# Performance work log

Measured on AMD Instinct MI355X. Metric: run time of the kernel, lower is better.

## Reference

```python
import jax, jax.numpy as jnp
import numpy as np

# Problem sizes
B, NPG, K = 64, 1024, 16          # graphs, nodes-per-graph, kNN neighbors
IN_CH, OUT_CH, SPACE, PROP = 64, 128, 4, 64
N = B * NPG


def setup_inputs() -> dict:
    key = jax.random.key(0)
    ks = jax.random.split(key, 10)

    def lin(k, out_d, in_d):
        return jax.random.normal(k, (out_d, in_d), jnp.float32) / np.sqrt(in_d)

    x = jax.random.normal(ks[0], (N, IN_CH), jnp.float32)
    z = jax.random.normal(ks[1], (N,), jnp.float32)
    batch = (jnp.arange(N) // NPG).astype(jnp.int32)  # 64 equal graphs
    return {
        "x": x,
        "z": z,
        "batch": batch,
        "Ws": lin(ks[2], SPACE, IN_CH),
        "bs": jnp.zeros((SPACE,), jnp.float32),
        "Wh": lin(ks[3], PROP, IN_CH),
        "bh": jnp.zeros((PROP,), jnp.float32),
        "Wskip": lin(ks[4], OUT_CH, IN_CH),
        "Wagg": lin(ks[5], OUT_CH, 4 * PROP),
        "bagg": jnp.zeros((OUT_CH,), jnp.float32),
        "gamma": jnp.ones((OUT_CH,), jnp.float32),
        "beta": jnp.zeros((OUT_CH,), jnp.float32),
    }


def reference(x, z, batch, Ws, bs, Wh, bh, Wskip, Wagg, bagg, gamma, beta):
    # --- linear projections (torch Linear: y = x @ W.T + b) ---
    s = x @ Ws.T + bs                              # [N, SPACE] learned space
    h = x @ Wh.T + bh                              # [N, PROP]  propagated feats

    sB = s.reshape(B, NPG, SPACE)
    hB = h.reshape(B, NPG, PROP)
    zB = z.reshape(B, NPG)

    # --- exact kNN per graph (knn_graph with batch, no self-loops) ---
    sq = jnp.sum(sB * sB, -1)                      # [B, n]
    d2 = sq[:, :, None] + sq[:, None, :] - 2.0 * jnp.einsum("bnd,bmd->bnm", sB, sB)
    d2 = jnp.where(jnp.eye(NPG, dtype=bool), jnp.inf, d2)  # exclude self
    _, idx = jax.lax.top_k(-d2, K)                 # idx[b, i, :] = k nearest j
    idx = jax.lax.stop_gradient(idx)

    gather = jax.vmap(lambda a, i: a[i])           # per-graph row gather

    # --- edge weights ew = exp(-10 * ||s_src - s_dst||^2) ---
    s_nb = gather(sB, idx)                         # [B, n, K, SPACE]
    ew = jnp.exp(-10.0 * jnp.sum((s_nb - sB[:, :, None, :]) ** 2, -1))  # [B,n,K]

    # --- messages m = h[src] * ew ; each dst has exactly K incoming edges ---
    m = gather(hB, idx) * ew[..., None]            # [B, n, K, PROP]
    agg_mean = m.mean(axis=2)                      # scatter_mean
    agg_max = m.max(axis=2)                        # scatter_max

    # --- DGN directional aggregations over Z ---
    dz = gather(zB, idx) - zB[:, :, None]          # z[src] - z[dst], [B,n,K]
    dz_abs_sum = jnp.sum(jnp.abs(dz), axis=2)      # scatter_sum(|dz|), [B,n]
    F = dz / (dz_abs_sum[:, :, None] + 1e-8)       # [B, n, K]
    agg_smooth = (m * jnp.abs(F)[..., None]).mean(axis=2)
    agg_deriv = (m * F[..., None]).sum(axis=2)

    agg = jnp.concatenate([agg_mean, agg_max, agg_smooth, agg_deriv], -1)
    agg = agg.reshape(N, 4 * PROP)

    out = x @ Wskip.T + (agg @ Wagg.T + bagg)      # [N, OUT_CH]

    # --- BatchNorm1d (training-mode batch stats, biased var) + ReLU ---
    mu = out.mean(axis=0)
    var = out.var(axis=0)
    out = gamma * (out - mu) * jax.lax.rsqrt(var + 1e-5) + beta
    return jax.nn.relu(out)
```

## Files before the change

### kernel.cpp

```cpp
#include <hip/hip_runtime.h>
#include <hip/hip_bf16.h>
#include <math.h>

#define NPG   1024
#define KNN   16
#define IN_CH 64
#define OUT_CH 128
#define SPACE 4
#define PROP  64
#define NGRAPH 64
#define NTOT  (NGRAPH*NPG)

typedef unsigned long long u64;
typedef unsigned int u32;

__global__ __launch_bounds__(256) void k1_proj(
    const float* __restrict__ x, const float* __restrict__ Ws, const float* __restrict__ bs,
    const float* __restrict__ Wh, const float* __restrict__ bh,
    float* __restrict__ s_out, float* __restrict__ h_out)
{
    __shared__ float whl[PROP*IN_CH];
    __shared__ float wsl[SPACE*IN_CH];
    int tid = threadIdx.x;
    {
        const float4* src = (const float4*)Wh;
        float4* dst = (float4*)whl;
        for (int e = tid; e < PROP*IN_CH/4; e += 256) dst[e] = src[e];
        if (tid < SPACE*IN_CH/4) ((float4*)wsl)[tid] = ((const float4*)Ws)[tid];
    }
    __syncthreads();
    int i = blockIdx.x*256 + tid;

    float4 xr[16];
    const float4* xrow = (const float4*)(x + (size_t)i*IN_CH);
    #pragma unroll
    for (int q = 0; q < 16; q++) xr[q] = xrow[q];

    #pragma unroll
    for (int d = 0; d < SPACE; d++) {
        float acc = bs[d];
        const float4* wr = (const float4*)(wsl + d*IN_CH);
        #pragma unroll
        for (int q = 0; q < 16; q++) {
            float4 w = wr[q];
            acc += xr[q].x*w.x + xr[q].y*w.y + xr[q].z*w.z + xr[q].w*w.w;
        }
        s_out[(size_t)i*SPACE + d] = acc;
    }
    #pragma unroll 4
    for (int p = 0; p < PROP; p++) {
        float acc = bh[p];
        const float4* wr = (const float4*)(whl + p*IN_CH);
        #pragma unroll
        for (int q = 0; q < 16; q++) {
            float4 w = wr[q];
            acc += xr[q].x*w.x + xr[q].y*w.y + xr[q].z*w.z + xr[q].w*w.w;
        }
        h_out[(size_t)i*PROP + p] = acc;
    }
}

#define MED3(d, x, a, b) asm("v_med3_u32 %0, %1, %2, %3" : "=v"(d) : "v"(x), "v"(a), "v"(b))
#define UMIN(a,b) ((a)<(b)?(a):(b))

#define INS16(x) do{ \
    u32 _x = (x); \
    MED3(kk15, _x, kk14, kk15); MED3(kk14, _x, kk13, kk14); \
    MED3(kk13, _x, kk12, kk13); MED3(kk12, _x, kk11, kk12); \
    MED3(kk11, _x, kk10, kk11); MED3(kk10, _x, kk9,  kk10); \
    MED3(kk9,  _x, kk8,  kk9 ); MED3(kk8,  _x, kk7,  kk8 ); \
    MED3(kk7,  _x, kk6,  kk7 ); MED3(kk6,  _x, kk5,  kk6 ); \
    MED3(kk5,  _x, kk4,  kk5 ); MED3(kk4,  _x, kk3,  kk4 ); \
    MED3(kk3,  _x, kk2,  kk3 ); MED3(kk2,  _x, kk1,  kk2 ); \
    MED3(kk1,  _x, kk0,  kk1 ); kk0 = UMIN(_x, kk0); \
}while(0)

#define CEU32(a,b) { u32 _lo = UMIN(a,b); u32 _hi = (a)<(b)?(b):(a); (a)=_lo; (b)=_hi; }
#define M16U(n0,n1,n2,n3,n4,n5,n6,n7,n8,n9,n10,n11,n12,n13,n14,n15) \
 CEU32(n0,n8) CEU32(n1,n9) CEU32(n2,n10) CEU32(n3,n11) CEU32(n4,n12) CEU32(n5,n13) CEU32(n6,n14) CEU32(n7,n15) \
 CEU32(n0,n4) CEU32(n1,n5) CEU32(n2,n6) CEU32(n3,n7) CEU32(n8,n12) CEU32(n9,n13) CEU32(n10,n14) CEU32(n11,n15) \
 CEU32(n0,n2) CEU32(n1,n3) CEU32(n4,n6) CEU32(n5,n7) CEU32(n8,n10) CEU32(n9,n11) CEU32(n12,n14) CEU32(n13,n15) \
 CEU32(n0,n1) CEU32(n2,n3) CEU32(n4,n5) CEU32(n6,n7) CEU32(n8,n9) CEU32(n10,n11) CEU32(n12,n13) CEU32(n14,n15)

#define MRGU(mm) do{ \
    u32 p0 =(u32)__shfl_xor((int)kk15,mm), p1 =(u32)__shfl_xor((int)kk14,mm); \
    u32 p2 =(u32)__shfl_xor((int)kk13,mm), p3 =(u32)__shfl_xor((int)kk12,mm); \
    u32 p4 =(u32)__shfl_xor((int)kk11,mm), p5 =(u32)__shfl_xor((int)kk10,mm); \
    u32 p6 =(u32)__shfl_xor((int)kk9, mm), p7 =(u32)__shfl_xor((int)kk8, mm); \
    u32 p8 =(u32)__shfl_xor((int)kk7, mm), p9 =(u32)__shfl_xor((int)kk6, mm); \
    u32 p10=(u32)__shfl_xor((int)kk5, mm), p11=(u32)__shfl_xor((int)kk4, mm); \
    u32 p12=(u32)__shfl_xor((int)kk3, mm), p13=(u32)__shfl_xor((int)kk2, mm); \
    u32 p14=(u32)__shfl_xor((int)kk1, mm), p15=(u32)__shfl_xor((int)kk0, mm); \
    kk0 =UMIN(kk0 ,p0 ); kk1 =UMIN(kk1 ,p1 ); kk2 =UMIN(kk2 ,p2 ); kk3 =UMIN(kk3 ,p3 ); \
    kk4 =UMIN(kk4 ,p4 ); kk5 =UMIN(kk5 ,p5 ); kk6 =UMIN(kk6 ,p6 ); kk7 =UMIN(kk7 ,p7 ); \
    kk8 =UMIN(kk8 ,p8 ); kk9 =UMIN(kk9 ,p9 ); kk10=UMIN(kk10,p10); kk11=UMIN(kk11,p11); \
    kk12=UMIN(kk12,p12); kk13=UMIN(kk13,p13); kk14=UMIN(kk14,p14); kk15=UMIN(kk15,p15); \
    M16U(kk0,kk1,kk2,kk3,kk4,kk5,kk6,kk7,kk8,kk9,kk10,kk11,kk12,kk13,kk14,kk15) \
}while(0)

#define OUTE8(e, kv) if (((e) & 7) == r) { \
    int _j = (int)((kv) & 1023u); \
    float4 _sj = s4[_j]; \
    float _dx = si.x-_sj.x, _dy = si.y-_sj.y, _dz = si.z-_sj.z, _dw = si.w-_sj.w; \
    float _d2 = _dx*_dx + _dy*_dy + _dz*_dz + _dw*_dw; \
    ew_out[bq + (e)] = expf(-10.0f * _d2); \
    idx_out[bq + (e)] = gbase + _j; }

__global__ __launch_bounds__(256) void k2_knn(
    const float* __restrict__ s, int* __restrict__ idx_out, float* __restrict__ ew_out)
{
    __shared__ float4 s4[NPG];
    int tid = threadIdx.x;
    int g     = blockIdx.x >> 5;
    int gbase = g * NPG;
    int qblk  = (blockIdx.x & 31) * 32;
    const float4* sg = (const float4*)(s + (size_t)g*NPG*SPACE);
    for (int e = tid; e < NPG; e += 256) s4[e] = sg[e];
    __syncthreads();

    int lane = tid & 63;
    int grp  = lane >> 3;
    int r    = lane & 7;
    int q    = qblk + (tid >> 6)*8 + grp;
    float4 si = s4[q];

    u32 kk0=~0u,kk1=~0u,kk2=~0u,kk3=~0u,kk4=~0u,kk5=~0u,kk6=~0u,kk7=~0u,
        kk8=~0u,kk9=~0u,kk10=~0u,kk11=~0u,kk12=~0u,kk13=~0u,kk14=~0u,kk15=~0u;

    int jb0 = r*128;
    #pragma unroll 2
    for (int it = 0; it < 128; ++it) {
        int j = jb0 + ((it + 3*r) & 127);
        float4 sj = s4[j];
        float dx = si.x-sj.x, dy = si.y-sj.y, dz = si.z-sj.z, dw = si.w-sj.w;
        float d2 = dx*dx + dy*dy + dz*dz + dw*dw;
        u32 key = (__float_as_uint(d2) & ~1023u) | (u32)j;
        key = (j == q) ? ~0u : key;
        INS16(key);
    }

    MRGU(1); MRGU(2); MRGU(4);

    size_t bq = ((size_t)(gbase + q)) * KNN;
    OUTE8(0,kk0)  OUTE8(1,kk1)  OUTE8(2,kk2)   OUTE8(3,kk3)
    OUTE8(4,kk4)  OUTE8(5,kk5)  OUTE8(6,kk6)   OUTE8(7,kk7)
    OUTE8(8,kk8)  OUTE8(9,kk9)  OUTE8(10,kk10) OUTE8(11,kk11)
    OUTE8(12,kk12) OUTE8(13,kk13) OUTE8(14,kk14) OUTE8(15,kk15)
}

typedef __attribute__((ext_vector_type(8))) short bf16x8;
typedef __attribute__((ext_vector_type(4))) float f32x4;

__device__ __forceinline__ u32 pk2bf(float a, float b) {
    u32 ua = __float_as_uint(a);
    u32 ub = __float_as_uint(b);
    ua = (ua + 0x7fffu + ((ua >> 16) & 1u)) >> 16;
    ub = (ub + 0x7fffu + ((ub >> 16) & 1u)) >> 16;
    return (ua & 0xffffu) | (ub << 16);
}
__device__ __forceinline__ unsigned short bfr(float a) {
    u32 ua = __float_as_uint(a);
    ua = (ua + 0x7fffu + ((ua >> 16) & 1u)) >> 16;
    return (unsigned short)ua;
}

__global__ __launch_bounds__(256) void k34_agg_gemm(
    const float* __restrict__ x, const float* __restrict__ h,
    const float* __restrict__ z, const int* __restrict__ idx,
    const float* __restrict__ ew,
    const float* __restrict__ Wskip, const float* __restrict__ Wagg,
    const float* __restrict__ bagg, float* __restrict__ out,
    float* __restrict__ partial)
{
    __shared__ char AggL[64*512];
    __shared__ char Bl[128*128];
    __shared__ float st[128], st2[128];
    int tid = threadIdx.x;
    int lane = tid & 63, wid = tid >> 6;
    int bid = blockIdx.x;
    int tile = (bid & 7) * 128 + (bid >> 3);
    int mbase = tile * 64;

    if (tid < 128) { st[tid] = 0.f; st2[tid] = 0.f; }

    #pragma unroll 2
    for (int t = 0; t < 16; ++t) {
        int row = wid*16 + t;
        int node = mbase + row;
        int kq = lane & 15;
        int jv = idx[(size_t)node*KNN + kq];
        float ev = ew[(size_t)node*KNN + kq];
        float dz = z[jv] - z[node];
        float as = fabsf(dz);
        as += __shfl_xor(as, 1); as += __shfl_xor(as, 2);
        as += __shfl_xor(as, 4); as += __shfl_xor(as, 8);
        float F = dz / (as + 1e-8f);
        float mean = 0.f, mx = -INFINITY, sm = 0.f, dv = 0.f;
        #pragma unroll
        for (int k = 0; k < KNN; ++k) {
            int   j = __shfl(jv, k);
            float e = __shfl(ev, k);
            float f = __shfl(F,  k);
            float hv = h[(size_t)j*PROP + lane];
            float m = hv * e;
            mean += m; mx = fmaxf(mx, m);
            sm += m * fabsf(f); dv += m * f;
        }
        int swz = (row & 7) << 4;
        char* rp = AggL + row*512;
        *(unsigned short*)(rp + ((2*(lane      )) ^ swz)) = bfr(mean * 0.0625f);
        *(unsigned short*)(rp + ((2*(lane +  64)) ^ swz)) = bfr(mx);
        *(unsigned short*)(rp + ((2*(lane + 128)) ^ swz)) = bfr(sm * 0.0625f);
        *(unsigned short*)(rp + ((2*(lane + 192)) ^ swz)) = bfr(dv);
    }

    int wy = wid >> 1, wx = wid & 1;
    int colb = wx*64 + (lane & 15);
    f32x4 acc[2][4];
    #pragma unroll
    for (int nc = 0; nc < 4; ++nc) {
        float bv = bagg[colb + nc*16];
        #pragma unroll
        for (int mr = 0; mr < 2; ++mr) acc[mr][nc] = (f32x4){bv, bv, bv, bv};
    }

    int brow = tid >> 1, bkq = (tid & 1) * 32;
    int bsw = (brow & 7) << 4;

    for (int ch = 0; ch < 5; ++ch) {
        __syncthreads();
        const float* bp = (ch == 0) ? (Wskip + (size_t)brow*64  + bkq)
                                    : (Wagg  + (size_t)brow*256 + (ch-1)*64 + bkq);
        #pragma unroll
        for (int g2 = 0; g2 < 4; ++g2) {
            float4 f0 = ((const float4*)bp)[2*g2], f1 = ((const float4*)bp)[2*g2+1];
            uint4 u = { pk2bf(f0.x,f0.y), pk2bf(f0.z,f0.w), pk2bf(f1.x,f1.y), pk2bf(f1.z,f1.w) };
            *(uint4*)(Bl + brow*128 + ((bkq*2 + g2*16) ^ bsw)) = u;
        }
        __syncthreads();

        #pragma unroll
        for (int ks = 0; ks < 2; ++ks) {
            int kb = ks*64 + ((lane >> 4) * 16);
            bf16x8 af[2], bfrg[4];
            if (ch == 0) {
                int ke = ks*32 + (lane >> 4)*8;
                #pragma unroll
                for (int mr = 0; mr < 2; ++mr) {
                    int row = mbase + wy*32 + mr*16 + (lane & 15);
                    const float* xp = x + (size_t)row*64 + ke;
                    float4 f0 = *(const float4*)xp, f1 = *(const float4*)(xp + 4);
                    union { u32 u[4]; bf16x8 v; } cv;
                    cv.u[0] = pk2bf(f0.x,f0.y); cv.u[1] = pk2bf(f0.z,f0.w);
                    cv.u[2] = pk2bf(f1.x,f1.y); cv.u[3] = pk2bf(f1.z,f1.w);
                    af[mr] = cv.v;
                }
            } else {
                #pragma unroll
                for (int mr = 0; mr < 2; ++mr) {
                    int row = wy*32 + mr*16 + (lane & 15);
                    af[mr] = *(const bf16x8*)(AggL + row*512 + (ch-1)*128
                                              + (kb ^ ((row & 7) << 4)));
                }
            }
            #pragma unroll
            for (int nc = 0; nc < 4; ++nc) {
                int n = wx*64 + nc*16 + (lane & 15);
                bfrg[nc] = *(const bf16x8*)(Bl + n*128 + (kb ^ ((n & 7) << 4)));
            }
            #pragma unroll
            for (int mr = 0; mr < 2; ++mr)
                #pragma unroll
                for (int nc = 0; nc < 4; ++nc)
                    acc[mr][nc] = __builtin_amdgcn_mfma_f32_16x16x32_bf16(
                        af[mr], bfrg[nc], acc[mr][nc], 0, 0, 0);
        }
    }

    float s1[4] = {0,0,0,0}, s2[4] = {0,0,0,0};
    #pragma unroll
    for (int mr = 0; mr < 2; ++mr) {
        int r0 = mbase + wy*32 + mr*16 + (lane >> 4)*4;
        #pragma unroll
        for (int nc = 0; nc < 4; ++nc) {
            int c = colb + nc*16;
            #pragma unroll
            for (int j = 0; j < 4; ++j) {
                float v = acc[mr][nc][j];
                out[(size_t)(r0 + j)*OUT_CH + c] = v;
                s1[nc] += v;
                s2[nc] += v*v;
            }
        }
    }
    #pragma unroll
    for (int nc = 0; nc < 4; ++nc) {
        s1[nc] += __shfl_xor(s1[nc], 16); s1[nc] += __shfl_xor(s1[nc], 32);
        s2[nc] += __shfl_xor(s2[nc], 16); s2[nc] += __shfl_xor(s2[nc], 32);
    }
    __syncthreads();
    if ((lane >> 4) == 0) {
        #pragma unroll
        for (int nc = 0; nc < 4; ++nc) {
            atomicAdd(&st[colb + nc*16],  s1[nc]);
            atomicAdd(&st2[colb + nc*16], s2[nc]);
        }
    }
    __syncthreads();
    if (tid < 128) {
        partial[(size_t)bid*256 + tid]       = st[tid];
        partial[(size_t)bid*256 + 128 + tid] = st2[tid];
    }
}

__global__ __launch_bounds__(256) void k5_red(
    const float* __restrict__ partial, float* __restrict__ sums)
{
    int c = threadIdx.x;
    int b0 = blockIdx.x * 32;
    float acc = 0.f;
    #pragma unroll 8
    for (int b = 0; b < 32; ++b)
        acc += partial[(size_t)(b0 + b)*256 + c];
    atomicAdd(&sums[c], acc);
}

__global__ __launch_bounds__(256) void k6_bn(
    float* __restrict__ out, const float* __restrict__ sums,
    const float* __restrict__ gamma, const float* __restrict__ beta)
{
    int f = blockIdx.x*256 + threadIdx.x;
    float4 v = *(float4*)(out + (size_t)f*4);
    int o0 = (f*4) & 127;
    const float invN = 1.f / (float)NTOT;
    float r[4] = {v.x, v.y, v.z, v.w};
    #pragma unroll
    for (int c = 0; c < 4; c++) {
        int o = o0 + c;
        float mu  = sums[o] * invN;
        float var = sums[128+o] * invN - mu*mu;
        float sc  = gamma[o] * rsqrtf(var + 1e-5f);
        float sh  = beta[o] - mu*sc;
        float y = r[c]*sc + sh;
        r[c] = y > 0.f ? y : 0.f;
    }
    *(float4*)(out + (size_t)f*4) = make_float4(r[0], r[1], r[2], r[3]);
}

extern "C" void kernel_launch(void* const* d_in, const int* in_sizes, int n_in,
                              void* d_out, int out_size, void* d_ws, size_t ws_size,
                              hipStream_t stream)
{
    (void)in_sizes; (void)n_in; (void)out_size; (void)ws_size;
    const float* x     = (const float*)d_in[0];
    const float* z     = (const float*)d_in[1];
    const float* Ws    = (const float*)d_in[3];
    const float* bs    = (const float*)d_in[4];
    const float* Wh    = (const float*)d_in[5];
    const float* bh    = (const float*)d_in[6];
    const float* Wskip = (const float*)d_in[7];
    const float* Wagg  = (const float*)d_in[8];
    const float* bagg  = (const float*)d_in[9];
    const float* gamma = (const float*)d_in[10];
    const float* beta  = (const float*)d_in[11];
    float* out = (float*)d_out;

    const size_t N = NTOT;
    float* ws   = (float*)d_ws;
    float* sbuf = ws;
    float* hbuf = sbuf + N*4;
    int*   idxb = (int*)(hbuf + N*64);
    float* ewb  = (float*)(idxb + N*16);
    float* part = ewb + N*16;
    float* sums = part + 1024*256;

    hipMemsetAsync(sums, 0, 256*sizeof(float), stream);
    k1_proj<<<NTOT/256, 256, 0, stream>>>(x, Ws, bs, Wh, bh, sbuf, hbuf);
    k2_knn <<<NGRAPH*32, 256, 0, stream>>>(sbuf, idxb, ewb);
    k34_agg_gemm<<<NTOT/64, 256, 0, stream>>>(x, hbuf, z, idxb, ewb,
                                              Wskip, Wagg, bagg, out, part);
    k5_red<<<32, 256, 0, stream>>>(part, sums);
    k6_bn <<<NTOT*OUT_CH/4/256, 256, 0, stream>>>(out, sums, gamma, beta);
}
```

Baseline: 269.0 us.

## Split fused aggregation+GEMM into separate gather kernel and bf16-staged GEMM

Un-fuses the neighbor aggregation from the MFMA GEMM kernel. A new k3_agg kernel runs one wavefront per node across 16K blocks and writes the 256-wide aggregated features as bf16 to a workspace buffer. The GEMM kernel then stages the x and aggregated tiles through LDS per K-chunk instead of holding a 32KB aggregated tile in LDS. This raises parallelism and occupancy for the latency-bound gather, and the smaller LDS footprint helps GEMM occupancy. In exchange it adds an extra kernel launch and a global round trip of 32MB of bf16 intermediates, and it drops the block swizzle that gave the gather L2 locality.

```diff
diff --git a/kernel.cpp b/kernel.cpp
--- a/kernel.cpp
+++ b/kernel.cpp
@@ -13,6 +13,7 @@
 
 typedef unsigned long long u64;
 typedef unsigned int u32;
+typedef unsigned short u16;
 
 __global__ __launch_bounds__(256) void k1_proj(
     const float* __restrict__ x, const float* __restrict__ Ws, const float* __restrict__ bs,
@@ -158,61 +159,64 @@
     ub = (ub + 0x7fffu + ((ub >> 16) & 1u)) >> 16;
     return (ua & 0xffffu) | (ub << 16);
 }
-__device__ __forceinline__ unsigned short bfr(float a) {
+__device__ __forceinline__ u16 bfr(float a) {
     u32 ua = __float_as_uint(a);
     ua = (ua + 0x7fffu + ((ua >> 16) & 1u)) >> 16;
-    return (unsigned short)ua;
-}
-
-__global__ __launch_bounds__(256) void k34_agg_gemm(
-    const float* __restrict__ x, const float* __restrict__ h,
-    const float* __restrict__ z, const int* __restrict__ idx,
-    const float* __restrict__ ew,
+    return (u16)ua;
+}
+
+__global__ __launch_bounds__(256) void k3_agg(
+    const float* __restrict__ h, const float* __restrict__ z,
+    const int* __restrict__ idx, const float* __restrict__ ew,
+    u16* __restrict__ agg16)
+{
+    int tid = threadIdx.x;
+    int lane = tid & 63;
+    int i = blockIdx.x*4 + (tid >> 6);
+    float zi = z[i];
+
+    int   kq = lane & 15;
+    int   jv = idx[(size_t)i*KNN + kq];
+    float ev = ew[(size_t)i*KNN + kq];
+    float dz = z[jv] - zi;
+    float as = fabsf(dz);
+    as += __shfl_xor(as, 1); as += __shfl_xor(as, 2);
+    as += __shfl_xor(as, 4); as += __shfl_xor(as, 8);
+    float F = dz / (as + 1e-8f);
+
+    float mean = 0.f, mx = -INFINITY, sm = 0.f, dv = 0.f;
+    #pragma unroll
+    for (int k = 0; k < KNN; ++k) {
+        int   j = __shfl(jv, k);
+        float e = __shfl(ev, k);
+        float f = __shfl(F,  k);
+        float hv = h[(size_t)j*PROP + lane];
+        float m = hv * e;
+        mean += m; mx = fmaxf(mx, m);
+        sm += m * fabsf(f); dv += m * f;
+    }
+    u16* ap = agg16 + (size_t)i*256;
+    ap[lane]       = bfr(mean * 0.0625f);
+    ap[64 + lane]  = bfr(mx);
+    ap[128 + lane] = bfr(sm * 0.0625f);
+    ap[192 + lane] = bfr(dv);
+}
+
+__global__ __launch_bounds__(256) void k4_gemm(
+    const float* __restrict__ x, const u16* __restrict__ agg16,
     const float* __restrict__ Wskip, const float* __restrict__ Wagg,
     const float* __restrict__ bagg, float* __restrict__ out,
     float* __restrict__ partial)
 {
-    __shared__ char AggL[64*512];
+    __shared__ char Atl[64*128];
     __shared__ char Bl[128*128];
     __shared__ float st[128], st2[128];
     int tid = threadIdx.x;
     int lane = tid & 63, wid = tid >> 6;
     int bid = blockIdx.x;
-    int tile = (bid & 7) * 128 + (bid >> 3);
-    int mbase = tile * 64;
+    int mbase = bid * 64;
 
     if (tid < 128) { st[tid] = 0.f; st2[tid] = 0.f; }
-
-    #pragma unroll 2
-    for (int t = 0; t < 16; ++t) {
-        int row = wid*16 + t;
-        int node = mbase + row;
-        int kq = lane & 15;
-        int jv = idx[(size_t)node*KNN + kq];
-        float ev = ew[(size_t)node*KNN + kq];
-        float dz = z[jv] - z[node];
-        float as = fabsf(dz);
-        as += __shfl_xor(as, 1); as += __shfl_xor(as, 2);
-        as += __shfl_xor(as, 4); as += __shfl_xor(as, 8);
-        float F = dz / (as + 1e-8f);
-        float mean = 0.f, mx = -INFINITY, sm = 0.f, dv = 0.f;
-        #pragma unroll
-        for (int k = 0; k < KNN; ++k) {
-            int   j = __shfl(jv, k);
-            float e = __shfl(ev, k);
-            float f = __shfl(F,  k);
-            float hv = h[(size_t)j*PROP + lane];
-            float m = hv * e;
-            mean += m; mx = fmaxf(mx, m);
-            sm += m * fabsf(f); dv += m * f;
-        }
-        int swz = (row & 7) << 4;
-        char* rp = AggL + row*512;
-        *(unsigned short*)(rp + ((2*(lane      )) ^ swz)) = bfr(mean * 0.0625f);
-        *(unsigned short*)(rp + ((2*(lane +  64)) ^ swz)) = bfr(mx);
-        *(unsigned short*)(rp + ((2*(lane + 128)) ^ swz)) = bfr(sm * 0.0625f);
-        *(unsigned short*)(rp + ((2*(lane + 192)) ^ swz)) = bfr(dv);
-    }
 
     int wy = wid >> 1, wx = wid & 1;
     int colb = wx*64 + (lane & 15);
@@ -224,11 +228,28 @@
         for (int mr = 0; mr < 2; ++mr) acc[mr][nc] = (f32x4){bv, bv, bv, bv};
     }
 
+    int arow = tid >> 2, aseg = (tid & 3) * 16;
+    int asw  = (arow & 7) << 4;
     int brow = tid >> 1, bkq = (tid & 1) * 32;
-    int bsw = (brow & 7) << 4;
+    int bsw  = (brow & 7) << 4;
 
     for (int ch = 0; ch < 5; ++ch) {
         __syncthreads();
+        if (ch == 0) {
+            const float* ap = x + (size_t)(mbase + arow)*64 + aseg;
+            float4 f0 = ((const float4*)ap)[0], f1 = ((const float4*)ap)[1];
+            float4 f2 = ((const float4*)ap)[2], f3 = ((const float4*)ap)[3];
+            uint4 u0 = { pk2bf(f0.x,f0.y), pk2bf(f0.z,f0.w), pk2bf(f1.x,f1.y), pk2bf(f1.z,f1.w) };
+            uint4 u1 = { pk2bf(f2.x,f2.y), pk2bf(f2.z,f2.w), pk2bf(f3.x,f3.y), pk2bf(f3.z,f3.w) };
+            *(uint4*)(Atl + arow*128 + ((aseg*2     ) ^ asw)) = u0;
+            *(uint4*)(Atl + arow*128 + ((aseg*2 + 16) ^ asw)) = u1;
+        } else {
+            const u16* ap = agg16 + (size_t)(mbase + arow)*256 + (ch-1)*64 + aseg;
+            uint4 u0 = ((const uint4*)ap)[0];
+            uint4 u1 = ((const uint4*)ap)[1];
+            *(uint4*)(Atl + arow*128 + ((aseg*2     ) ^ asw)) = u0;
+            *(uint4*)(Atl + arow*128 + ((aseg*2 + 16) ^ asw)) = u1;
+        }
         const float* bp = (ch == 0) ? (Wskip + (size_t)brow*64  + bkq)
                                     : (Wagg  + (size_t)brow*256 + (ch-1)*64 + bkq);
         #pragma unroll
@@ -243,25 +264,10 @@
         for (int ks = 0; ks < 2; ++ks) {
             int kb = ks*64 + ((lane >> 4) * 16);
             bf16x8 af[2], bfrg[4];
-            if (ch == 0) {
-                int ke = ks*32 + (lane >> 4)*8;
-                #pragma unroll
-                for (int mr = 0; mr < 2; ++mr) {
-                    int row = mbase + wy*32 + mr*16 + (lane & 15);
-                    const float* xp = x + (size_t)row*64 + ke;
-                    float4 f0 = *(const float4*)xp, f1 = *(const float4*)(xp + 4);
-                    union { u32 u[4]; bf16x8 v; } cv;
-                    cv.u[0] = pk2bf(f0.x,f0.y); cv.u[1] = pk2bf(f0.z,f0.w);
-                    cv.u[2] = pk2bf(f1.x,f1.y); cv.u[3] = pk2bf(f1.z,f1.w);
-                    af[mr] = cv.v;
-                }
-            } else {
-                #pragma unroll
-                for (int mr = 0; mr < 2; ++mr) {
-                    int row = wy*32 + mr*16 + (lane & 15);
-                    af[mr] = *(const bf16x8*)(AggL + row*512 + (ch-1)*128
-                                              + (kb ^ ((row & 7) << 4)));
-                }
+            #pragma unroll
+            for (int mr = 0; mr < 2; ++mr) {
+                int row = wy*32 + mr*16 + (lane & 15);
+                af[mr] = *(const bf16x8*)(Atl + row*128 + (kb ^ ((row & 7) << 4)));
             }
             #pragma unroll
             for (int nc = 0; nc < 4; ++nc) {
@@ -366,19 +372,20 @@
     float* out = (float*)d_out;
 
     const size_t N = NTOT;
-    float* ws   = (float*)d_ws;
-    float* sbuf = ws;
-    float* hbuf = sbuf + N*4;
-    int*   idxb = (int*)(hbuf + N*64);
-    float* ewb  = (float*)(idxb + N*16);
-    float* part = ewb + N*16;
-    float* sums = part + 1024*256;
+    float* ws    = (float*)d_ws;
+    float* sbuf  = ws;
+    float* hbuf  = sbuf + N*4;
+    int*   idxb  = (int*)(hbuf + N*64);
+    float* ewb   = (float*)(idxb + N*16);
+    u16*   agg16 = (u16*)(ewb + N*16);
+    float* part  = (float*)(agg16 + N*256);
+    float* sums  = part + 1024*256;
 
     hipMemsetAsync(sums, 0, 256*sizeof(float), stream);
     k1_proj<<<NTOT/256, 256, 0, stream>>>(x, Ws, bs, Wh, bh, sbuf, hbuf);
     k2_knn <<<NGRAPH*32, 256, 0, stream>>>(sbuf, idxb, ewb);
-    k34_agg_gemm<<<NTOT/64, 256, 0, stream>>>(x, hbuf, z, idxb, ewb,
-                                              Wskip, Wagg, bagg, out, part);
-    k5_red<<<32, 256, 0, stream>>>(part, sums);
-    k6_bn <<<NTOT*OUT_CH/4/256, 256, 0, stream>>>(out, sums, gamma, beta);
-}
+    k3_agg <<<NTOT/4,   256, 0, stream>>>(hbuf, z, idxb, ewb, agg16);
+    k4_gemm<<<NTOT/64,  256, 0, stream>>>(x, agg16, Wskip, Wagg, bagg, out, part);
+    k5_red <<<32, 256, 0, stream>>>(part, sums);
+    k6_bn  <<<NTOT*OUT_CH/4/256, 256, 0, stream>>>(out, sums, gamma, beta);
+}
```

New measurement: 265.4 us. No clear change (-1.4%).
